# Kernel optimization log

Measured on AMD Instinct MI355X. Metric: run time of the kernel, lower is better.

The kernel has to match this reference:

```python
import jax, jax.numpy as jnp
import numpy as np

N = 100000
E = 1600000
IN_DIM = 128
HID = 128
LABELS = 64
EPS = 1e-5


def setup_inputs() -> dict:
    key = jax.random.key(0)
    ks = jax.random.split(key, 20)
    x = jax.random.normal(ks[0], (N, IN_DIM), dtype=jnp.float32)
    edge_index = jax.random.randint(ks[1], (2, E), 0, N, dtype=jnp.int64)
    edge_weight = jax.random.uniform(ks[2], (E,), dtype=jnp.float32)
    def lin(k, fi, fo):
        s = 1.0 / np.sqrt(fi)
        return jax.random.uniform(k, (fi, fo), jnp.float32, -s, s)
    inp = {
        "x": x, "edge_index": edge_index, "edge_weight": edge_weight,
        "W1": lin(ks[3], IN_DIM, HID), "b1": jnp.zeros((HID,), jnp.float32),
        "g1": jnp.ones((HID,), jnp.float32), "be1": jnp.zeros((HID,), jnp.float32),
        "W2": lin(ks[4], HID, HID), "b2": jnp.zeros((HID,), jnp.float32),
        "g2": jnp.ones((HID,), jnp.float32), "be2": jnp.zeros((HID,), jnp.float32),
        "W3": lin(ks[5], HID, HID), "b3": jnp.zeros((HID,), jnp.float32),
        "g3": jnp.ones((HID,), jnp.float32), "be3": jnp.zeros((HID,), jnp.float32),
        "Wh": lin(ks[6], HID, LABELS),
        "bh": jnp.zeros((LABELS,), jnp.float32),
    }
    return inp


def _gcn_norm(edge_index, edge_weight):
    # PyG GCNConv: add self-loops (weight 1), symmetric normalization.
    self_idx = jnp.arange(N, dtype=edge_index.dtype)
    row = jnp.concatenate([edge_index[0], self_idx])   # source
    col = jnp.concatenate([edge_index[1], self_idx])   # target
    w = jnp.concatenate([edge_weight, jnp.ones((N,), edge_weight.dtype)])
    deg = jax.ops.segment_sum(w, col, num_segments=N)  # in-degree with self loops
    dinv = jnp.where(deg > 0, jax.lax.rsqrt(deg), 0.0)
    norm = dinv[row] * w * dinv[col]                   # [E+N]
    return row, col, norm


def _gcn_conv(x, row, col, norm, W, b):
    h = x @ W                                           # [N, F] transform first (PyG order)
    msg = h[row] * norm[:, None]                        # gather + scale  [E+N, F]
    out = jax.ops.segment_sum(msg, col, num_segments=N) # scatter-add at targets
    return out + b


def _bn(h, g, be):
    # BatchNorm1d over nodes (training-mode batch statistics, biased var)
    mu = jnp.mean(h, axis=0)
    var = jnp.mean(jnp.square(h - mu), axis=0)
    return (h - mu) * jax.lax.rsqrt(var + EPS) * g + be


def reference(x, edge_index, edge_weight, W1, b1, g1, be1, W2, b2, g2, be2,
              W3, b3, g3, be3, Wh, bh):
    row, col, norm = _gcn_norm(edge_index, edge_weight)
    h1 = jax.nn.relu(_bn(_gcn_conv(x, row, col, norm, W1, b1), g1, be1))
    h2 = jax.nn.relu(_bn(_gcn_conv(h1, row, col, norm, W2, b2), g2, be2) + h1)
    h3 = jax.nn.relu(_bn(_gcn_conv(h2, row, col, norm, W3, b3), g3, be3) + h2)
    return h3 @ Wh + bh
```

## Files before the change

### kernel.cpp

```cpp
#include <hip/hip_runtime.h>


typedef unsigned long long u64;
#define DEG_MASK 0xFFFFFFFFFFFFULL
#define WSCALE 2147483648.0f

__global__ void detect_i64(const int* __restrict__ ei32, int* __restrict__ flag) {
  int lane = threadIdx.x & 63;
  int v = ei32[2 * lane + 1];
  unsigned long long b = __ballot(v == 0);
  if (lane == 0) *flag = (b == ~0ull) ? 1 : 0;
}

__global__ __launch_bounds__(256) void init_k(u64* __restrict__ packed,
                                              float* __restrict__ stats, int n) {
  int i = blockIdx.x * 256 + threadIdx.x;
  if (i < n) packed[i] = 0ull;
  if (i < 768) stats[i] = 0.0f;
}

__global__ __launch_bounds__(256) void edge_hist(const int* __restrict__ ei32,
                                                 const float* __restrict__ w,
                                                 u64* __restrict__ packed,
                                                 unsigned short* __restrict__ rank,
                                                 const int* __restrict__ flag, int e) {
  int i = blockIdx.x * 256 + threadIdx.x;
  if (i >= e) return;
  int is64 = *flag;
  int c = is64 ? ei32[2 * (e + i)] : ei32[e + i];
  u64 add = ((u64)1 << 48) | (u64)(unsigned)__float2uint_rn(w[i] * WSCALE);
  u64 old = atomicAdd(&packed[c], add);
  rank[i] = (unsigned short)(old >> 48);
}

__global__ __launch_bounds__(256) void scan_blocksum(const u64* __restrict__ packed,
                                                     int* __restrict__ bsum, int n) {
  __shared__ int s[256];
  int i = blockIdx.x * 256 + threadIdx.x;
  s[threadIdx.x] = (i < n) ? (int)(packed[i] >> 48) : 0;
  __syncthreads();
  for (int off = 128; off > 0; off >>= 1) {
    if (threadIdx.x < off) s[threadIdx.x] += s[threadIdx.x + off];
    __syncthreads();
  }
  if (threadIdx.x == 0) bsum[blockIdx.x] = s[0];
}

__global__ __launch_bounds__(256) void scan_small(int* __restrict__ bsum, int nb) {
  __shared__ int s[256];
  __shared__ int carry_s;
  if (threadIdx.x == 0) carry_s = 0;
  __syncthreads();
  for (int base = 0; base < nb; base += 256) {
    int idx = base + threadIdx.x;
    int v = (idx < nb) ? bsum[idx] : 0;
    s[threadIdx.x] = v;
    __syncthreads();
    for (int off = 1; off < 256; off <<= 1) {
      int t = (threadIdx.x >= (unsigned)off) ? s[threadIdx.x - off] : 0;
      __syncthreads();
      s[threadIdx.x] += t;
      __syncthreads();
    }
    int carry = carry_s;
    if (idx < nb) bsum[idx] = carry + s[threadIdx.x] - v;
    __syncthreads();
    if (threadIdx.x == 255) carry_s = carry + s[255];
    __syncthreads();
  }
}

__global__ __launch_bounds__(256) void scan_final(const u64* __restrict__ packed,
                                                  const int* __restrict__ boff,
                                                  int* __restrict__ rowptr,
                                                  float* __restrict__ dinv,
                                                  int n, int e_total) {
  __shared__ int s[256];
  int i = blockIdx.x * 256 + threadIdx.x;
  u64 p = (i < n) ? packed[i] : 0ull;
  int v = (int)(p >> 48);
  s[threadIdx.x] = v;
  __syncthreads();
  for (int off = 1; off < 256; off <<= 1) {
    int t = (threadIdx.x >= (unsigned)off) ? s[threadIdx.x - off] : 0;
    __syncthreads();
    s[threadIdx.x] += t;
    __syncthreads();
  }
  if (i < n) {
    rowptr[i] = boff[blockIdx.x] + s[threadIdx.x] - v;
    float deg = 1.0f + (float)(p & DEG_MASK) * (1.0f / WSCALE);
    dinv[i] = rsqrtf(deg);
  }
  if (i == 0) rowptr[n] = e_total;
}

__global__ __launch_bounds__(256) void edge_fill(const int* __restrict__ ei32,
                                                 const float* __restrict__ w,
                                                 const float* __restrict__ dinv,
                                                 const int* __restrict__ rowptr,
                                                 const unsigned short* __restrict__ rank,
                                                 int2* __restrict__ csr,
                                                 const int* __restrict__ flag, int e) {
  int i = blockIdx.x * 256 + threadIdx.x;
  if (i >= e) return;
  int is64 = *flag;
  int r, c;
  if (is64) { r = ei32[2 * i]; c = ei32[2 * (e + i)]; }
  else      { r = ei32[i];     c = ei32[e + i]; }
  float nrm = dinv[r] * w[i] * dinv[c];
  int pos = rowptr[c] + (int)rank[i];
  csr[pos] = make_int2(r, __float_as_int(nrm));
}

template <int CPT>
__global__ __launch_bounds__(256) void gemm_k128(const float* __restrict__ A,
                                                 const float* __restrict__ W,
                                                 const float* __restrict__ bias,
                                                 float* __restrict__ out, int n) {
  constexpr int OC = 32 * CPT;
  __shared__ float As[64][128];
  const int tid = threadIdx.x;
  const int r0 = blockIdx.x * 64;
  #pragma unroll
  for (int i = 0; i < 8; ++i) {
    int idx = tid + i * 256;
    int row = idx >> 5;
    int c4 = (idx & 31) << 2;
    float4 v = make_float4(0.f, 0.f, 0.f, 0.f);
    int gr = r0 + row;
    if (gr < n) v = *reinterpret_cast<const float4*>(&A[(size_t)gr * 128 + c4]);
    *reinterpret_cast<float4*>(&As[row][c4]) = v;
  }
  __syncthreads();

  const int lc = (tid & 31) * CPT;
  const int lr = (tid >> 5) * 8;
  float acc[8][CPT];
  #pragma unroll
  for (int i = 0; i < 8; ++i)
    #pragma unroll
    for (int j = 0; j < CPT; ++j) acc[i][j] = 0.f;

  #pragma unroll 2
  for (int k4 = 0; k4 < 128; k4 += 4) {
    float a[8][4];
    #pragma unroll
    for (int i = 0; i < 8; ++i) {
      float4 t = *reinterpret_cast<const float4*>(&As[lr + i][k4]);
      a[i][0] = t.x; a[i][1] = t.y; a[i][2] = t.z; a[i][3] = t.w;
    }
    #pragma unroll
    for (int kk = 0; kk < 4; ++kk) {
      float wv[CPT];
      const float* wrow = &W[(size_t)(k4 + kk) * OC + lc];
      if constexpr (CPT == 4) {
        float4 t = *reinterpret_cast<const float4*>(wrow);
        wv[0] = t.x; wv[1] = t.y; wv[2] = t.z; wv[3] = t.w;
      } else {
        float2 t = *reinterpret_cast<const float2*>(wrow);
        wv[0] = t.x; wv[1] = t.y;
      }
      #pragma unroll
      for (int i = 0; i < 8; ++i)
        #pragma unroll
        for (int j = 0; j < CPT; ++j)
          acc[i][j] = fmaf(a[i][kk], wv[j], acc[i][j]);
    }
  }

  float bv[CPT];
  #pragma unroll
  for (int j = 0; j < CPT; ++j) bv[j] = bias ? bias[lc + j] : 0.f;
  #pragma unroll
  for (int i = 0; i < 8; ++i) {
    int gr = r0 + lr + i;
    if (gr < n) {
      if constexpr (CPT == 4) {
        float4 o = make_float4(acc[i][0] + bv[0], acc[i][1] + bv[1],
                               acc[i][2] + bv[2], acc[i][3] + bv[3]);
        *reinterpret_cast<float4*>(&out[(size_t)gr * OC + lc]) = o;
      } else {
        float2 o = make_float2(acc[i][0] + bv[0], acc[i][1] + bv[1]);
        *reinterpret_cast<float2*>(&out[(size_t)gr * OC + lc]) = o;
      }
    }
  }
}

__global__ __launch_bounds__(256) void gcn_gather(const float* __restrict__ h,
                                                  const int* __restrict__ rowptr,
                                                  const int2* __restrict__ csr,
                                                  const float* __restrict__ dinv,
                                                  const float* __restrict__ bias,
                                                  float* __restrict__ out, int n) {
  int wave = threadIdx.x >> 6;
  int lane = threadIdx.x & 63;
  int node = blockIdx.x * 4 + wave;
  if (node >= n) return;
  const float2* hp = reinterpret_cast<const float2*>(h);
  float di = dinv[node];
  float2 hv = hp[(size_t)node * 64 + lane];
  float s = di * di;
  float ax = s * hv.x, ay = s * hv.y;
  int e0 = rowptr[node], e1 = rowptr[node + 1];
  int e = e0;
  for (; e + 3 < e1; e += 4) {
    int2 pa = csr[e];
    int2 pb = csr[e + 1];
    int2 pc = csr[e + 2];
    int2 pd = csr[e + 3];
    float2 sa = hp[(size_t)pa.x * 64 + lane];
    float2 sb = hp[(size_t)pb.x * 64 + lane];
    float2 sc = hp[(size_t)pc.x * 64 + lane];
    float2 sd = hp[(size_t)pd.x * 64 + lane];
    float na = __int_as_float(pa.y), nb = __int_as_float(pb.y);
    float nc = __int_as_float(pc.y), nd = __int_as_float(pd.y);
    ax = fmaf(na, sa.x, ax); ay = fmaf(na, sa.y, ay);
    ax = fmaf(nb, sb.x, ax); ay = fmaf(nb, sb.y, ay);
    ax = fmaf(nc, sc.x, ax); ay = fmaf(nc, sc.y, ay);
    ax = fmaf(nd, sd.x, ax); ay = fmaf(nd, sd.y, ay);
  }
  for (; e < e1; ++e) {
    int2 p = csr[e];
    float2 sv = hp[(size_t)p.x * 64 + lane];
    float nm = __int_as_float(p.y);
    ax = fmaf(nm, sv.x, ax); ay = fmaf(nm, sv.y, ay);
  }
  int f = lane * 2;
  float bx = bias ? bias[f] : 0.f;
  float by = bias ? bias[f + 1] : 0.f;
  float2 o = make_float2(ax + bx, ay + by);
  reinterpret_cast<float2*>(out)[(size_t)node * 64 + lane] = o;
}

__global__ __launch_bounds__(256) void bn_stats(const float* __restrict__ h,
                                                float* __restrict__ stats, int n) {
  int f = threadIdx.x & 127;
  int half = threadIdx.x >> 7;
  float s = 0.f, q = 0.f;
  for (int r = blockIdx.x * 2 + half; r < n; r += gridDim.x * 2) {
    float v = h[(size_t)r * 128 + f];
    s += v;
    q = fmaf(v, v, q);
  }
  __shared__ float ls[256], lq[256];
  ls[threadIdx.x] = s; lq[threadIdx.x] = q;
  __syncthreads();
  if (half == 0) {
    s += ls[threadIdx.x + 128];
    q += lq[threadIdx.x + 128];
    atomicAdd(&stats[f], s);
    atomicAdd(&stats[128 + f], q);
  }
}

__global__ void bn_finalize(const float* __restrict__ stats,
                            const float* __restrict__ g,
                            const float* __restrict__ be,
                            float* __restrict__ scsh, float inv_n) {
  int f = threadIdx.x;
  float mean = stats[f] * inv_n;
  float var = stats[128 + f] * inv_n - mean * mean;
  float sc = g[f] * rsqrtf(var + 1e-5f);
  scsh[f] = sc;
  scsh[128 + f] = be[f] - mean * sc;
}

template <bool RES>
__global__ __launch_bounds__(256) void bn_apply(const float* __restrict__ c,
                                                const float* __restrict__ res,
                                                const float* __restrict__ scsh,
                                                float* __restrict__ out, int n4) {
  int i = blockIdx.x * 256 + threadIdx.x;
  if (i >= n4) return;
  int f4 = (i & 31) * 4;
  float4 v = reinterpret_cast<const float4*>(c)[i];
  float4 sc = *reinterpret_cast<const float4*>(&scsh[f4]);
  float4 sh = *reinterpret_cast<const float4*>(&scsh[128 + f4]);
  float4 o;
  o.x = fmaf(v.x, sc.x, sh.x);
  o.y = fmaf(v.y, sc.y, sh.y);
  o.z = fmaf(v.z, sc.z, sh.z);
  o.w = fmaf(v.w, sc.w, sh.w);
  if (RES) {
    float4 r = reinterpret_cast<const float4*>(res)[i];
    o.x += r.x; o.y += r.y; o.z += r.z; o.w += r.w;
  }
  o.x = fmaxf(o.x, 0.f); o.y = fmaxf(o.y, 0.f);
  o.z = fmaxf(o.z, 0.f); o.w = fmaxf(o.w, 0.f);
  reinterpret_cast<float4*>(out)[i] = o;
}

extern "C" void kernel_launch(void* const* d_in, const int* in_sizes, int n_in,
                              void* d_out, int out_size, void* d_ws, size_t ws_size,
                              hipStream_t stream) {
  const float* x   = (const float*)d_in[0];
  const int*   ei  = (const int*)d_in[1];
  const float* ew  = (const float*)d_in[2];
  const float* W1  = (const float*)d_in[3];
  const float* b1  = (const float*)d_in[4];
  const float* g1  = (const float*)d_in[5];
  const float* be1 = (const float*)d_in[6];
  const float* W2  = (const float*)d_in[7];
  const float* b2  = (const float*)d_in[8];
  const float* g2  = (const float*)d_in[9];
  const float* be2 = (const float*)d_in[10];
  const float* W3  = (const float*)d_in[11];
  const float* b3  = (const float*)d_in[12];
  const float* g3  = (const float*)d_in[13];
  const float* be3 = (const float*)d_in[14];
  const float* Wh  = (const float*)d_in[15];
  const float* bh  = (const float*)d_in[16];

  const int N = in_sizes[0] / 128;
  const int E = in_sizes[2];

  char* base = (char*)d_ws;
  size_t off = 0;
  auto alloc = [&](size_t bytes) -> void* {
    off = (off + 511) & ~size_t(511);
    void* p = base + off;
    off += bytes;
    return p;
  };
  int*            flag   = (int*)alloc(4);
  u64*            packed = (u64*)alloc((size_t)N * 8);
  float*          dinv   = (float*)alloc((size_t)N * 4);
  int*            rowptr = (int*)alloc((size_t)(N + 1) * 4);
  int*            bsum   = (int*)alloc(1024 * 4);
  float*          stats  = (float*)alloc(768 * 4);
  float*          scsh   = (float*)alloc(256 * 4);
  unsigned short* rank   = (unsigned short*)alloc((size_t)E * 2);
  int2*           csr    = (int2*)alloc((size_t)E * 8);
  float*          X0     = (float*)alloc((size_t)N * 128 * 4);
  float*          X1     = (float*)alloc((size_t)N * 128 * 4);
  float*          X2     = (float*)alloc((size_t)N * 128 * 4);
  (void)ws_size; (void)n_in; (void)out_size;

  const int nb = (N + 255) / 256;
  const int eb = (E + 255) / 256;
  const int gb = (N + 63) / 64;
  const int cb = (N + 3) / 4;
  const int ab = (N * 32 + 255) / 256;

  detect_i64<<<1, 64, 0, stream>>>(ei, flag);
  init_k<<<nb, 256, 0, stream>>>(packed, stats, N);
  edge_hist<<<eb, 256, 0, stream>>>(ei, ew, packed, rank, flag, E);
  scan_blocksum<<<nb, 256, 0, stream>>>(packed, bsum, N);
  scan_small<<<1, 256, 0, stream>>>(bsum, nb);
  scan_final<<<nb, 256, 0, stream>>>(packed, bsum, rowptr, dinv, N, E);
  edge_fill<<<eb, 256, 0, stream>>>(ei, ew, dinv, rowptr, rank, csr, flag, E);

  gemm_k128<4><<<gb, 256, 0, stream>>>(x, W1, (const float*)nullptr, X0, N);
  gcn_gather<<<cb, 256, 0, stream>>>(X0, rowptr, csr, dinv, b1, X1, N);
  bn_stats<<<512, 256, 0, stream>>>(X1, stats + 0, N);
  bn_finalize<<<1, 128, 0, stream>>>(stats + 0, g1, be1, scsh, 1.0f / N);
  bn_apply<false><<<ab, 256, 0, stream>>>(X1, (const float*)nullptr, scsh, X2, N * 32);

  gemm_k128<4><<<gb, 256, 0, stream>>>(X2, W2, (const float*)nullptr, X0, N);
  gcn_gather<<<cb, 256, 0, stream>>>(X0, rowptr, csr, dinv, b2, X1, N);
  bn_stats<<<512, 256, 0, stream>>>(X1, stats + 256, N);
  bn_finalize<<<1, 128, 0, stream>>>(stats + 256, g2, be2, scsh, 1.0f / N);
  bn_apply<true><<<ab, 256, 0, stream>>>(X1, X2, scsh, X0, N * 32);

  gemm_k128<4><<<gb, 256, 0, stream>>>(X0, W3, (const float*)nullptr, X1, N);
  gcn_gather<<<cb, 256, 0, stream>>>(X1, rowptr, csr, dinv, b3, X2, N);
  bn_stats<<<512, 256, 0, stream>>>(X2, stats + 512, N);
  bn_finalize<<<1, 128, 0, stream>>>(stats + 512, g3, be3, scsh, 1.0f / N);
  bn_apply<true><<<ab, 256, 0, stream>>>(X2, X0, scsh, X1, N * 32);

  gemm_k128<2><<<gb, 256, 0, stream>>>(X1, Wh, bh, (float*)d_out, N);
}
```

Measured before the change: 988.3 us.

## Fuse BN stats into gather and BN apply/residual/ReLU into next GEMM load

The gather kernel now runs a persistent grid-stride loop over nodes and accumulates per-feature sum and sum-of-squares, replacing the separate bn_stats pass. The BN scale/shift, residual add and ReLU are applied while loading the next GEMM's A tile, so the bn_apply kernels and their full-tensor read/write passes are gone. Layer 3's GEMM writes the recomputed h2 back in place to serve as the residual for the head. The cost is extra ALU work per GEMM load and a fixed 2048-block gather grid, which may affect load balance.

```diff
diff --git a/kernel.cpp b/kernel.cpp
--- a/kernel.cpp
+++ b/kernel.cpp
@@ -113,24 +113,66 @@
   csr[pos] = make_int2(r, __float_as_int(nrm));
 }
 
-template <int CPT>
-__global__ __launch_bounds__(256) void gemm_k128(const float* __restrict__ A,
-                                                 const float* __restrict__ W,
-                                                 const float* __restrict__ bias,
-                                                 float* __restrict__ out, int n) {
+template <int CPT, int MODE>
+__global__ __launch_bounds__(256) void gemm_k128f(const float* A0, const float* A1,
+                                                  const float* __restrict__ scsh0,
+                                                  const float* __restrict__ scsh1,
+                                                  float* side,
+                                                  const float* __restrict__ W,
+                                                  const float* __restrict__ bias,
+                                                  float* __restrict__ out, int n) {
   constexpr int OC = 32 * CPT;
   __shared__ float As[64][128];
   const int tid = threadIdx.x;
   const int r0 = blockIdx.x * 64;
+  const int c4s = (tid & 31) << 2;
+  float4 sc0, sh0, sc1, sh1;
+  if (MODE == 1 || MODE == 2) {
+    sc0 = *reinterpret_cast<const float4*>(&scsh0[c4s]);
+    sh0 = *reinterpret_cast<const float4*>(&scsh0[128 + c4s]);
+  }
+  if (MODE == 2 || MODE == 3) {
+    sc1 = *reinterpret_cast<const float4*>(&scsh1[c4s]);
+    sh1 = *reinterpret_cast<const float4*>(&scsh1[128 + c4s]);
+  }
   #pragma unroll
   for (int i = 0; i < 8; ++i) {
     int idx = tid + i * 256;
     int row = idx >> 5;
-    int c4 = (idx & 31) << 2;
+    int gr = r0 + row;
     float4 v = make_float4(0.f, 0.f, 0.f, 0.f);
-    int gr = r0 + row;
-    if (gr < n) v = *reinterpret_cast<const float4*>(&A[(size_t)gr * 128 + c4]);
-    *reinterpret_cast<float4*>(&As[row][c4]) = v;
+    if (gr < n) {
+      size_t base = (size_t)gr * 128 + c4s;
+      if (MODE == 0) {
+        v = *reinterpret_cast<const float4*>(&A0[base]);
+      } else if (MODE == 1) {
+        float4 a = *reinterpret_cast<const float4*>(&A0[base]);
+        v.x = fmaxf(fmaf(a.x, sc0.x, sh0.x), 0.f);
+        v.y = fmaxf(fmaf(a.y, sc0.y, sh0.y), 0.f);
+        v.z = fmaxf(fmaf(a.z, sc0.z, sh0.z), 0.f);
+        v.w = fmaxf(fmaf(a.w, sc0.w, sh0.w), 0.f);
+      } else if (MODE == 2) {
+        float4 a = *reinterpret_cast<const float4*>(&A0[base]);
+        float4 b = *reinterpret_cast<const float4*>(&A1[base]);
+        float hx = fmaxf(fmaf(a.x, sc0.x, sh0.x), 0.f);
+        float hy = fmaxf(fmaf(a.y, sc0.y, sh0.y), 0.f);
+        float hz = fmaxf(fmaf(a.z, sc0.z, sh0.z), 0.f);
+        float hw = fmaxf(fmaf(a.w, sc0.w, sh0.w), 0.f);
+        v.x = fmaxf(fmaf(b.x, sc1.x, sh1.x) + hx, 0.f);
+        v.y = fmaxf(fmaf(b.y, sc1.y, sh1.y) + hy, 0.f);
+        v.z = fmaxf(fmaf(b.z, sc1.z, sh1.z) + hz, 0.f);
+        v.w = fmaxf(fmaf(b.w, sc1.w, sh1.w) + hw, 0.f);
+        *reinterpret_cast<float4*>(&side[base]) = v;
+      } else {
+        float4 a = *reinterpret_cast<const float4*>(&A0[base]);
+        float4 b = *reinterpret_cast<const float4*>(&A1[base]);
+        v.x = fmaxf(fmaf(b.x, sc1.x, sh1.x) + a.x, 0.f);
+        v.y = fmaxf(fmaf(b.y, sc1.y, sh1.y) + a.y, 0.f);
+        v.z = fmaxf(fmaf(b.z, sc1.z, sh1.z) + a.z, 0.f);
+        v.w = fmaxf(fmaf(b.w, sc1.w, sh1.w) + a.w, 0.f);
+      }
+    }
+    *reinterpret_cast<float4*>(&As[row][c4s]) = v;
   }
   __syncthreads();
 
@@ -193,65 +235,68 @@
                                                   const int2* __restrict__ csr,
                                                   const float* __restrict__ dinv,
                                                   const float* __restrict__ bias,
-                                                  float* __restrict__ out, int n) {
-  int wave = threadIdx.x >> 6;
-  int lane = threadIdx.x & 63;
-  int node = blockIdx.x * 4 + wave;
-  if (node >= n) return;
+                                                  float* __restrict__ out,
+                                                  float* __restrict__ stats, int n) {
+  const int wave = threadIdx.x >> 6;
+  const int lane = threadIdx.x & 63;
   const float2* hp = reinterpret_cast<const float2*>(h);
-  float di = dinv[node];
-  float2 hv = hp[(size_t)node * 64 + lane];
-  float s = di * di;
-  float ax = s * hv.x, ay = s * hv.y;
-  int e0 = rowptr[node], e1 = rowptr[node + 1];
-  int e = e0;
-  for (; e + 3 < e1; e += 4) {
-    int2 pa = csr[e];
-    int2 pb = csr[e + 1];
-    int2 pc = csr[e + 2];
-    int2 pd = csr[e + 3];
-    float2 sa = hp[(size_t)pa.x * 64 + lane];
-    float2 sb = hp[(size_t)pb.x * 64 + lane];
-    float2 sc = hp[(size_t)pc.x * 64 + lane];
-    float2 sd = hp[(size_t)pd.x * 64 + lane];
-    float na = __int_as_float(pa.y), nb = __int_as_float(pb.y);
-    float nc = __int_as_float(pc.y), nd = __int_as_float(pd.y);
-    ax = fmaf(na, sa.x, ax); ay = fmaf(na, sa.y, ay);
-    ax = fmaf(nb, sb.x, ax); ay = fmaf(nb, sb.y, ay);
-    ax = fmaf(nc, sc.x, ax); ay = fmaf(nc, sc.y, ay);
-    ax = fmaf(nd, sd.x, ax); ay = fmaf(nd, sd.y, ay);
-  }
-  for (; e < e1; ++e) {
-    int2 p = csr[e];
-    float2 sv = hp[(size_t)p.x * 64 + lane];
-    float nm = __int_as_float(p.y);
-    ax = fmaf(nm, sv.x, ax); ay = fmaf(nm, sv.y, ay);
-  }
-  int f = lane * 2;
-  float bx = bias ? bias[f] : 0.f;
-  float by = bias ? bias[f + 1] : 0.f;
-  float2 o = make_float2(ax + bx, ay + by);
-  reinterpret_cast<float2*>(out)[(size_t)node * 64 + lane] = o;
-}
-
-__global__ __launch_bounds__(256) void bn_stats(const float* __restrict__ h,
-                                                float* __restrict__ stats, int n) {
-  int f = threadIdx.x & 127;
-  int half = threadIdx.x >> 7;
-  float s = 0.f, q = 0.f;
-  for (int r = blockIdx.x * 2 + half; r < n; r += gridDim.x * 2) {
-    float v = h[(size_t)r * 128 + f];
-    s += v;
-    q = fmaf(v, v, q);
-  }
-  __shared__ float ls[256], lq[256];
-  ls[threadIdx.x] = s; lq[threadIdx.x] = q;
-  __syncthreads();
-  if (half == 0) {
-    s += ls[threadIdx.x + 128];
-    q += lq[threadIdx.x + 128];
-    atomicAdd(&stats[f], s);
-    atomicAdd(&stats[128 + f], q);
+  const int f = lane * 2;
+  const float bx = bias[f], by = bias[f + 1];
+  float s0 = 0.f, q0 = 0.f, s1 = 0.f, q1 = 0.f;
+
+  for (int node = blockIdx.x * 4 + wave; node < n; node += gridDim.x * 4) {
+    float di = dinv[node];
+    float2 hv = hp[(size_t)node * 64 + lane];
+    float sw = di * di;
+    float ax = sw * hv.x, ay = sw * hv.y;
+    int e0 = rowptr[node], e1 = rowptr[node + 1];
+    int e = e0;
+    for (; e + 3 < e1; e += 4) {
+      int2 pa = csr[e];
+      int2 pb = csr[e + 1];
+      int2 pc = csr[e + 2];
+      int2 pd = csr[e + 3];
+      float2 sa = hp[(size_t)pa.x * 64 + lane];
+      float2 sb = hp[(size_t)pb.x * 64 + lane];
+      float2 sc = hp[(size_t)pc.x * 64 + lane];
+      float2 sd = hp[(size_t)pd.x * 64 + lane];
+      float na = __int_as_float(pa.y), nb = __int_as_float(pb.y);
+      float nc = __int_as_float(pc.y), nd = __int_as_float(pd.y);
+      ax = fmaf(na, sa.x, ax); ay = fmaf(na, sa.y, ay);
+      ax = fmaf(nb, sb.x, ax); ay = fmaf(nb, sb.y, ay);
+      ax = fmaf(nc, sc.x, ax); ay = fmaf(nc, sc.y, ay);
+      ax = fmaf(nd, sd.x, ax); ay = fmaf(nd, sd.y, ay);
+    }
+    for (; e < e1; ++e) {
+      int2 p = csr[e];
+      float2 sv = hp[(size_t)p.x * 64 + lane];
+      float nm = __int_as_float(p.y);
+      ax = fmaf(nm, sv.x, ax); ay = fmaf(nm, sv.y, ay);
+    }
+    float ox = ax + bx, oy = ay + by;
+    reinterpret_cast<float2*>(out)[(size_t)node * 64 + lane] = make_float2(ox, oy);
+    s0 += ox; q0 = fmaf(ox, ox, q0);
+    s1 += oy; q1 = fmaf(oy, oy, q1);
+  }
+
+  __shared__ float red[4][256];
+  red[wave][lane * 4 + 0] = s0;
+  red[wave][lane * 4 + 1] = q0;
+  red[wave][lane * 4 + 2] = s1;
+  red[wave][lane * 4 + 3] = q1;
+  __syncthreads();
+  if (wave == 0) {
+    #pragma unroll
+    for (int w = 1; w < 4; ++w) {
+      s0 += red[w][lane * 4 + 0];
+      q0 += red[w][lane * 4 + 1];
+      s1 += red[w][lane * 4 + 2];
+      q1 += red[w][lane * 4 + 3];
+    }
+    atomicAdd(&stats[f], s0);
+    atomicAdd(&stats[128 + f], q0);
+    atomicAdd(&stats[f + 1], s1);
+    atomicAdd(&stats[128 + f + 1], q1);
   }
 }
 
@@ -265,31 +310,6 @@
   float sc = g[f] * rsqrtf(var + 1e-5f);
   scsh[f] = sc;
   scsh[128 + f] = be[f] - mean * sc;
-}
-
-template <bool RES>
-__global__ __launch_bounds__(256) void bn_apply(const float* __restrict__ c,
-                                                const float* __restrict__ res,
-                                                const float* __restrict__ scsh,
-                                                float* __restrict__ out, int n4) {
-  int i = blockIdx.x * 256 + threadIdx.x;
-  if (i >= n4) return;
-  int f4 = (i & 31) * 4;
-  float4 v = reinterpret_cast<const float4*>(c)[i];
-  float4 sc = *reinterpret_cast<const float4*>(&scsh[f4]);
-  float4 sh = *reinterpret_cast<const float4*>(&scsh[128 + f4]);
-  float4 o;
-  o.x = fmaf(v.x, sc.x, sh.x);
-  o.y = fmaf(v.y, sc.y, sh.y);
-  o.z = fmaf(v.z, sc.z, sh.z);
-  o.w = fmaf(v.w, sc.w, sh.w);
-  if (RES) {
-    float4 r = reinterpret_cast<const float4*>(res)[i];
-    o.x += r.x; o.y += r.y; o.z += r.z; o.w += r.w;
-  }
-  o.x = fmaxf(o.x, 0.f); o.y = fmaxf(o.y, 0.f);
-  o.z = fmaxf(o.z, 0.f); o.w = fmaxf(o.w, 0.f);
-  reinterpret_cast<float4*>(out)[i] = o;
 }
 
 extern "C" void kernel_launch(void* const* d_in, const int* in_sizes, int n_in,
@@ -324,25 +344,24 @@
     off += bytes;
     return p;
   };
-  int*            flag   = (int*)alloc(4);
-  u64*            packed = (u64*)alloc((size_t)N * 8);
-  float*          dinv   = (float*)alloc((size_t)N * 4);
-  int*            rowptr = (int*)alloc((size_t)(N + 1) * 4);
-  int*            bsum   = (int*)alloc(1024 * 4);
-  float*          stats  = (float*)alloc(768 * 4);
-  float*          scsh   = (float*)alloc(256 * 4);
-  unsigned short* rank   = (unsigned short*)alloc((size_t)E * 2);
-  int2*           csr    = (int2*)alloc((size_t)E * 8);
-  float*          X0     = (float*)alloc((size_t)N * 128 * 4);
-  float*          X1     = (float*)alloc((size_t)N * 128 * 4);
-  float*          X2     = (float*)alloc((size_t)N * 128 * 4);
+  int*            flag    = (int*)alloc(4);
+  u64*            packed  = (u64*)alloc((size_t)N * 8);
+  float*          dinv    = (float*)alloc((size_t)N * 4);
+  int*            rowptr  = (int*)alloc((size_t)(N + 1) * 4);
+  int*            bsum    = (int*)alloc(1024 * 4);
+  float*          stats   = (float*)alloc(768 * 4);
+  float*          scshAll = (float*)alloc(768 * 4);
+  unsigned short* rank    = (unsigned short*)alloc((size_t)E * 2);
+  int2*           csr     = (int2*)alloc((size_t)E * 8);
+  float*          P       = (float*)alloc((size_t)N * 128 * 4);
+  float*          Q       = (float*)alloc((size_t)N * 128 * 4);
+  float*          R       = (float*)alloc((size_t)N * 128 * 4);
   (void)ws_size; (void)n_in; (void)out_size;
 
   const int nb = (N + 255) / 256;
   const int eb = (E + 255) / 256;
   const int gb = (N + 63) / 64;
-  const int cb = (N + 3) / 4;
-  const int ab = (N * 32 + 255) / 256;
+  const int cb = 2048;
 
   detect_i64<<<1, 64, 0, stream>>>(ei, flag);
   init_k<<<nb, 256, 0, stream>>>(packed, stats, N);
@@ -352,23 +371,21 @@
   scan_final<<<nb, 256, 0, stream>>>(packed, bsum, rowptr, dinv, N, E);
   edge_fill<<<eb, 256, 0, stream>>>(ei, ew, dinv, rowptr, rank, csr, flag, E);
 
-  gemm_k128<4><<<gb, 256, 0, stream>>>(x, W1, (const float*)nullptr, X0, N);
-  gcn_gather<<<cb, 256, 0, stream>>>(X0, rowptr, csr, dinv, b1, X1, N);
-  bn_stats<<<512, 256, 0, stream>>>(X1, stats + 0, N);
-  bn_finalize<<<1, 128, 0, stream>>>(stats + 0, g1, be1, scsh, 1.0f / N);
-  bn_apply<false><<<ab, 256, 0, stream>>>(X1, (const float*)nullptr, scsh, X2, N * 32);
-
-  gemm_k128<4><<<gb, 256, 0, stream>>>(X2, W2, (const float*)nullptr, X0, N);
-  gcn_gather<<<cb, 256, 0, stream>>>(X0, rowptr, csr, dinv, b2, X1, N);
-  bn_stats<<<512, 256, 0, stream>>>(X1, stats + 256, N);
-  bn_finalize<<<1, 128, 0, stream>>>(stats + 256, g2, be2, scsh, 1.0f / N);
-  bn_apply<true><<<ab, 256, 0, stream>>>(X1, X2, scsh, X0, N * 32);
-
-  gemm_k128<4><<<gb, 256, 0, stream>>>(X0, W3, (const float*)nullptr, X1, N);
-  gcn_gather<<<cb, 256, 0, stream>>>(X1, rowptr, csr, dinv, b3, X2, N);
-  bn_stats<<<512, 256, 0, stream>>>(X2, stats + 512, N);
-  bn_finalize<<<1, 128, 0, stream>>>(stats + 512, g3, be3, scsh, 1.0f / N);
-  bn_apply<true><<<ab, 256, 0, stream>>>(X2, X0, scsh, X1, N * 32);
-
-  gemm_k128<2><<<gb, 256, 0, stream>>>(X1, Wh, bh, (float*)d_out, N);
-}
+  gemm_k128f<4, 0><<<gb, 256, 0, stream>>>(x, nullptr, nullptr, nullptr, nullptr,
+                                           W1, nullptr, P, N);
+  gcn_gather<<<cb, 256, 0, stream>>>(P, rowptr, csr, dinv, b1, Q, stats + 0, N);
+  bn_finalize<<<1, 128, 0, stream>>>(stats + 0, g1, be1, scshAll + 0, 1.0f / N);
+
+  gemm_k128f<4, 1><<<gb, 256, 0, stream>>>(Q, nullptr, scshAll + 0, nullptr, nullptr,
+                                           W2, nullptr, P, N);
+  gcn_gather<<<cb, 256, 0, stream>>>(P, rowptr, csr, dinv, b2, R, stats + 256, N);
+  bn_finalize<<<1, 128, 0, stream>>>(stats + 256, g2, be2, scshAll + 256, 1.0f / N);
+
+  gemm_k128f<4, 2><<<gb, 256, 0, stream>>>(Q, R, scshAll + 0, scshAll + 256, Q,
+                                           W3, nullptr, P, N);
+  gcn_gather<<<cb, 256, 0, stream>>>(P, rowptr, csr, dinv, b3, R, stats + 512, N);
+  bn_finalize<<<1, 128, 0, stream>>>(stats + 512, g3, be3, scshAll + 512, 1.0f / N);
+
+  gemm_k128f<2, 3><<<gb, 256, 0, stream>>>(Q, R, nullptr, scshAll + 512, nullptr,
+                                           Wh, bh, (float*)d_out, N);
+}
```

New measurement: 1.085 ms. 1.1x slower.
